# Performance work log

Measured on AMD Instinct MI355X. Metric: run time of the kernel, lower is better.

Reference implementation:

```python
import jax, jax.numpy as jnp
import numpy as np

N = 50000      # nodes
E = 1_600_000  # edges (avg degree 32)
IN = 256
HID = 64
H = 4          # heads
OUT = 128
NEG = 0.2      # LeakyReLU negative slope


def setup_inputs() -> dict:
    key = jax.random.key(0)
    ks = jax.random.split(key, 16)
    def p(i, shape):
        return jax.random.normal(ks[i], shape, jnp.float32) * 0.05
    x = jax.random.normal(ks[0], (N, IN), jnp.float32)
    edge_index = jax.random.randint(ks[1], (2, E), 0, N, dtype=jnp.int64)
    return dict(
        x=x, edge_index=edge_index,
        W0=p(2, (IN, H * HID)), as0=p(3, (H, HID)), ad0=p(4, (H, HID)), b0=p(5, (H * HID,)),
        W1=p(6, (H * HID, H * HID)), as1=p(7, (H, HID)), ad1=p(8, (H, HID)), b1=p(9, (H * HID,)),
        W2=p(10, (H * HID, OUT)), as2=p(11, (1, OUT)), ad2=p(12, (1, OUT)), b2=p(13, (OUT,)),
        Wl=p(14, (H * HID, OUT)), bl=p(15, (OUT,)),
    )


def gat_conv(x, src, dst, W, a_s, a_d, b, heads, ch):
    # Linear projection -> per-head features [N, H, C]
    h = (x @ W).reshape(-1, heads, ch)
    # Per-node attention logits [N, H]
    al_s = jnp.einsum('nhc,hc->nh', h, a_s)
    al_d = jnp.einsum('nhc,hc->nh', h, a_d)
    # Per-edge logits: gather + LeakyReLU  [E2, H]
    e = jax.nn.leaky_relu(al_s[src] + al_d[dst], NEG)
    # Segment softmax over destination neighborhoods (stable)
    m = jax.ops.segment_max(e, dst, num_segments=N)
    e = jnp.exp(e - m[dst])
    s = jax.ops.segment_sum(e, dst, num_segments=N)
    a = e / s[dst]
    # Weighted scatter-add aggregation [N, H, C]
    out = jax.ops.segment_sum(a[:, :, None] * h[src], dst, num_segments=N)
    return out.reshape(N, heads * ch) + b


def reference(x, edge_index, W0, as0, ad0, b0, W1, as1, ad1, b1, W2, as2, ad2, b2, Wl, bl):
    # add self-loops (PyG GATConv default)
    loop = jnp.arange(N, dtype=edge_index.dtype)
    src = jnp.concatenate([edge_index[0], loop])
    dst = jnp.concatenate([edge_index[1], loop])
    # layer 0: in -> hid*heads (no residual at layer 0)
    h0 = gat_conv(x, src, dst, W0, as0, ad0, b0, H, HID)
    # layer 1: hid*heads -> hid*heads, residual
    h1 = gat_conv(h0, src, dst, W1, as1, ad1, b1, H, HID) + h0
    # layer 2 (last): hid*heads -> out with 1 head, residual via last_linear
    h2 = gat_conv(h1, src, dst, W2, as2, ad2, b2, 1, OUT) + (h1 @ Wl + bl)
    return h2
```

## Files before the change

### kernel.cpp

```cpp
#include <hip/hip_runtime.h>
#include <hip/hip_bf16.h>

#define N_NODES 50000
#define N_EDGES 1600000
#define E2 (N_EDGES + N_NODES)
#define NB 782
#define BCAP 3072
#define CHUNK 8192
#define NBLK_E 202
#define NS 7
#define RP2W 8

typedef __attribute__((ext_vector_type(8))) short bf16x8;
typedef __attribute__((ext_vector_type(4))) float f32x4;

static __device__ __forceinline__ float lrelu(float x) { return x > 0.f ? x : 0.2f * x; }

static __device__ __forceinline__ float b2f(ushort u) {
    union { unsigned int u; float f; } v;
    v.u = ((unsigned int)u) << 16;
    return v.f;
}
static __device__ __forceinline__ float hi2f(unsigned int u) {
    union { unsigned int u; float f; } v;
    v.u = u & 0xffff0000u;
    return v.f;
}
static __device__ __forceinline__ float lo2f(unsigned int u) {
    union { unsigned int u; float f; } v;
    v.u = u << 16;
    return v.f;
}
static __device__ __forceinline__ ushort f2b(float f) {
    union { float f; unsigned int u; } v;
    v.f = f;
    unsigned int r = v.u + 0x7FFFu + ((v.u >> 16) & 1u);
    return (ushort)(r >> 16);
}


__global__ __launch_bounds__(256) void k_bhist(const int* __restrict__ edst, int* __restrict__ hist) {
    __shared__ int cnt[NB];
    int t = threadIdx.x;
    for (int i = t; i < NB; i += 256) cnt[i] = 0;
    __syncthreads();
    int e0 = blockIdx.x * CHUNK;
    int eend = min(e0 + CHUNK, E2);
    for (int e = e0 + t; e < eend; e += 256) {
        int d = (e < N_EDGES) ? edst[e] : (e - N_EDGES);
        atomicAdd(&cnt[d >> 6], 1);
    }
    __syncthreads();
    for (int i = t; i < NB; i += 256) hist[blockIdx.x * NB + i] = cnt[i];
}

__global__ __launch_bounds__(1024) void k_colscan(const int* __restrict__ hist,
                                                  int* __restrict__ start, int* __restrict__ btotal) {
    int b = threadIdx.x;
    if (b >= NB) return;
    int run = 0;
#pragma unroll 4
    for (int blk = 0; blk < NBLK_E; ++blk) {
        int v = hist[blk * NB + b];
        start[blk * NB + b] = run;
        run += v;
    }
    btotal[b] = run;
}

__global__ __launch_bounds__(256) void k_bscan(const int* __restrict__ btotal, int* __restrict__ bbase) {
    __shared__ int s[256];
    int t = threadIdx.x;
    int v[4];
    int sum = 0;
#pragma unroll
    for (int k = 0; k < 4; ++k) {
        int i = t * 4 + k;
        v[k] = (i < NB) ? btotal[i] : 0;
        sum += v[k];
    }
    s[t] = sum;
    __syncthreads();
    for (int off = 1; off < 256; off <<= 1) {
        int add = (t >= off) ? s[t - off] : 0;
        __syncthreads();
        s[t] += add;
        __syncthreads();
    }
    int base = s[t] - sum;
#pragma unroll
    for (int k = 0; k < 4; ++k) {
        int i = t * 4 + k;
        if (i < NB) bbase[i] = base;
        base += v[k];
    }
}

__global__ __launch_bounds__(256) void k_bscatter(const int* __restrict__ esrc, const int* __restrict__ edst,
                                                  const int* __restrict__ start, const int* __restrict__ bbase,
                                                  unsigned int* __restrict__ bbuf) {
    __shared__ int cnt[NB];
    __shared__ int cur[NB];
    __shared__ int gofs[NB];
    __shared__ int s_scan[256];
    __shared__ unsigned int s_e[CHUNK];
    int t = threadIdx.x;
    for (int i = t; i < NB; i += 256) cnt[i] = 0;
    __syncthreads();
    int e0 = blockIdx.x * CHUNK;
    int eend = min(e0 + CHUNK, E2);
    for (int e = e0 + t; e < eend; e += 256) {
        int d = (e < N_EDGES) ? edst[e] : (e - N_EDGES);
        atomicAdd(&cnt[d >> 6], 1);
    }
    __syncthreads();
    int v[4];
    int sum = 0;
#pragma unroll
    for (int k = 0; k < 4; ++k) {
        int i = t * 4 + k;
        v[k] = (i < NB) ? cnt[i] : 0;
        sum += v[k];
    }
    s_scan[t] = sum;
    __syncthreads();
    for (int off = 1; off < 256; off <<= 1) {
        int add = (t >= off) ? s_scan[t - off] : 0;
        __syncthreads();
        s_scan[t] += add;
        __syncthreads();
    }
    int run = s_scan[t] - sum;
#pragma unroll
    for (int k = 0; k < 4; ++k) {
        int i = t * 4 + k;
        if (i < NB) {
            cur[i] = run;
            gofs[i] = bbase[i] + start[blockIdx.x * NB + i] - run;
        }
        run += v[k];
    }
    __syncthreads();
    for (int e = e0 + t; e < eend; e += 256) {
        int s, d;
        if (e < N_EDGES) { s = esrc[e]; d = edst[e]; } else { s = d = e - N_EDGES; }
        int b = d >> 6;
        int pos = atomicAdd(&cur[b], 1);
        s_e[pos] = (unsigned int)s | ((unsigned int)(d & 63) << 16) | ((unsigned int)b << 22);
    }
    __syncthreads();
    int cntall = eend - e0;
    for (int i = t; i < cntall; i += 256) {
        unsigned int p = s_e[i];
        int b = p >> 22;
        bbuf[gofs[b] + i] = p & 0x3FFFFFu;
    }
}

__global__ __launch_bounds__(256) void k_build(const int* __restrict__ btotal, const int* __restrict__ bbase,
                                               const unsigned int* __restrict__ bbuf,
                                               int* __restrict__ rowptr2, int* __restrict__ col) {
    const int b = blockIdx.x;
    const int t = threadIdx.x;
    const int cnt = btotal[b];
    const int base = bbase[b];
    const int node0 = b << 6;

    __shared__ unsigned int s_e[BCAP];
    __shared__ int s_cnt[512];
    __shared__ int s_cur[512];
    __shared__ int s_scan[256];

    s_cnt[t] = 0; s_cnt[t + 256] = 0;
    __syncthreads();
    for (int i = t; i < cnt; i += 256) {
        unsigned int p = bbuf[(size_t)base + i];
        s_e[i] = p;
        int key = (int)((p >> 16) & 63) * 8 + (int)((p & 0xFFFFu) >> 13);
        atomicAdd(&s_cnt[key], 1);
    }
    __syncthreads();
    int v0 = s_cnt[t * 2], v1 = s_cnt[t * 2 + 1];
    int sum = v0 + v1;
    s_scan[t] = sum;
    __syncthreads();
    for (int off = 1; off < 256; off <<= 1) {
        int add = (t >= off) ? s_scan[t - off] : 0;
        __syncthreads();
        s_scan[t] += add;
        __syncthreads();
    }
    int run = s_scan[t] - sum;
    s_cur[t * 2] = run;
    s_cur[t * 2 + 1] = run + v0;
    __syncthreads();
    {
        int key0 = t * 2, key1 = t * 2 + 1;
        int n0 = node0 + (key0 >> 3);
        int n1 = node0 + (key1 >> 3);
        if (n0 < N_NODES) rowptr2[(size_t)n0 * RP2W + (key0 & 7)] = base + s_cur[key0];
        if (n1 < N_NODES) rowptr2[(size_t)n1 * RP2W + (key1 & 7)] = base + s_cur[key1];
    }
    __syncthreads();
    for (int i = t; i < cnt; i += 256) {
        unsigned int p = s_e[i];
        int key = (int)((p >> 16) & 63) * 8 + (int)((p & 0xFFFFu) >> 13);
        int pos = atomicAdd(&s_cur[key], 1);
        col[base + pos] = (int)(p & 0xFFFFu);
    }
}


__global__ void k_quant(const float* __restrict__ x, ushort* __restrict__ xb, int n4) {
    int i = blockIdx.x * 256 + threadIdx.x;
    if (i >= n4) return;
    float4 v = ((const float4*)x)[i];
    ushort4 o;
    o.x = f2b(v.x); o.y = f2b(v.y); o.z = f2b(v.z); o.w = f2b(v.w);
    ((ushort4*)xb)[i] = o;
}

__global__ void k_wprep(const float* __restrict__ W0, const float* __restrict__ W1,
                        const float* __restrict__ W2, const float* __restrict__ Wl,
                        ushort* __restrict__ Wt0, ushort* __restrict__ Wt1, ushort* __restrict__ Wtc) {
    int g = blockIdx.x * 256 + threadIdx.x;
    int sec = g >> 16;
    int i = g & 0xFFFF;
    int k = i >> 8, n = i & 255;
    if (sec == 0) {
        Wt0[n * 256 + k] = f2b(W0[i]);
    } else if (sec == 1) {
        Wt1[n * 256 + k] = f2b(W1[i]);
    } else {
        float v = (n < 128) ? W2[k * 128 + n] : Wl[k * 128 + (n - 128)];
        Wtc[n * 256 + k] = f2b(v);
    }
}


template <bool FUSE>
__global__ __launch_bounds__(256) void k_mfma(const ushort* __restrict__ A, const ushort* __restrict__ Bt,
                                              ushort* __restrict__ Cb, int M,
                                              const float* __restrict__ a_s, const float* __restrict__ a_d,
                                              float* __restrict__ als, float* __restrict__ ald) {
    const int t = threadIdx.x;
    const int w = t >> 6, l = t & 63;
    const int lr = l & 15, lk = l >> 4;
    const int m0 = blockIdx.x * 32;
    const int n0 = w * 64;
    f32x4 acc[2][4] = {};

    int r0 = m0 + lr;      if (r0 >= M) r0 = M - 1;
    int r1 = m0 + 16 + lr; if (r1 >= M) r1 = M - 1;
    const ushort* a0p = A + (size_t)r0 * 256 + lk * 8;
    const ushort* a1p = A + (size_t)r1 * 256 + lk * 8;
    const ushort* bp  = Bt + (size_t)(n0 + lr) * 256 + lk * 8;

#pragma unroll
    for (int k0 = 0; k0 < 256; k0 += 32) {
        bf16x8 a0 = *(const bf16x8*)(a0p + k0);
        bf16x8 a1 = *(const bf16x8*)(a1p + k0);
#pragma unroll
        for (int n = 0; n < 4; ++n) {
            bf16x8 b = *(const bf16x8*)(bp + n * 16 * 256 + k0);
            acc[0][n] = __builtin_amdgcn_mfma_f32_16x16x32_bf16(a0, b, acc[0][n], 0, 0, 0);
            acc[1][n] = __builtin_amdgcn_mfma_f32_16x16x32_bf16(a1, b, acc[1][n], 0, 0, 0);
        }
    }

#pragma unroll
    for (int m = 0; m < 2; ++m) {
#pragma unroll
        for (int r = 0; r < 4; ++r) {
            int row = m0 + m * 16 + lk * 4 + r;
            if (row >= M) continue;
#pragma unroll
            for (int n = 0; n < 4; ++n) {
                Cb[(size_t)row * 256 + n0 + n * 16 + lr] = f2b(acc[m][n][r]);
            }
        }
    }

    if constexpr (FUSE) {
        float asc[4], adc[4];
#pragma unroll
        for (int n = 0; n < 4; ++n) {
            int c = n0 + n * 16 + lr;
            asc[n] = a_s[c];
            adc[n] = a_d[c];
        }
#pragma unroll
        for (int m = 0; m < 2; ++m) {
#pragma unroll
            for (int r = 0; r < 4; ++r) {
                float pa = 0.f, pd = 0.f;
#pragma unroll
                for (int n = 0; n < 4; ++n) {
                    pa += acc[m][n][r] * asc[n];
                    pd += acc[m][n][r] * adc[n];
                }
#pragma unroll
                for (int off = 1; off < 16; off <<= 1) {
                    pa += __shfl_xor(pa, off);
                    pd += __shfl_xor(pd, off);
                }
                if (lr == 0) {
                    int row = m0 + m * 16 + lk * 4 + r;
                    if (row < M) {
                        als[row * 4 + w] = pa;
                        ald[row * 4 + w] = pd;
                    }
                }
            }
        }
    }
}


template <int HEADS, int CHAN>
__global__ __launch_bounds__(256) void k_al(const ushort* __restrict__ Pb,
                                            const float* __restrict__ a_s, const float* __restrict__ a_d,
                                            float* __restrict__ als, float* __restrict__ ald) {
    int n = blockIdx.x * 4 + (threadIdx.x >> 6);
    if (n >= N_NODES) return;
    int l = threadIdx.x & 63;
    const ushort* row = Pb + (size_t)n * 256;
#pragma unroll
    for (int h = 0; h < HEADS; ++h) {
        float ps = 0.f, pd = 0.f;
#pragma unroll
        for (int c = l; c < CHAN; c += 64) {
            float v = b2f(row[h * CHAN + c]);
            ps += v * a_s[h * CHAN + c];
            pd += v * a_d[h * CHAN + c];
        }
#pragma unroll
        for (int off = 32; off > 0; off >>= 1) {
            ps += __shfl_xor(ps, off);
            pd += __shfl_xor(pd, off);
        }
        if (l == 0) { als[n * HEADS + h] = ps; ald[n * HEADS + h] = pd; }
    }
}


template <int HEADS>
__device__ __forceinline__ void load_als(const float* __restrict__ als, int src, float* v) {
    if constexpr (HEADS == 4) {
        float4 a = *(const float4*)(als + (size_t)src * 4);
        v[0] = a.x; v[1] = a.y; v[2] = a.z; v[3] = a.w;
    } else {
        v[0] = als[src];
    }
}


template <int HEADS, int CHAN, bool RESB, bool LIN, bool WRITEF, bool WRITEB>
__global__ __launch_bounds__(256) void k_aggw(
    const ushort* __restrict__ Pb,
    const float* __restrict__ als, const float* __restrict__ ald,
    const int* __restrict__ rowptr2, const int* __restrict__ col,
    const float* __restrict__ bias, const float* __restrict__ bias2,
    const ushort* __restrict__ residb, float* __restrict__ out, ushort* __restrict__ outb) {
    constexpr int BLK = HEADS * CHAN;
    constexpr int CPL = BLK / 64;
    const int t = threadIdx.x;
    const int w = t >> 6, l = t & 63;
    const int n = blockIdx.x * 4 + w;
    const int rs = rowptr2[(size_t)n * RP2W];
    const int deg = rowptr2[(size_t)n * RP2W + NS] - rs;

    __shared__ int s_src[4][64];
    __shared__ float s_w[4][64 * HEADS];

    float aldn[HEADS];
    load_als<HEADS>(ald, n, aldn);

    float acc[CPL];
#pragma unroll
    for (int c = 0; c < CPL; ++c) acc[c] = 0.f;
    float sw[HEADS];
#pragma unroll
    for (int h = 0; h < HEADS; ++h) sw[h] = 0.f;

    const int hsel = l >> 4;

    for (int base = 0; base < deg; base += 64) {
        int j = base + l;
        if (j < deg) {
            int src = col[rs + j];
            s_src[w][l] = src;
            float av[HEADS];
            load_als<HEADS>(als, src, av);
#pragma unroll
            for (int h = 0; h < HEADS; ++h) {
                float wv = __expf(lrelu(av[h] + aldn[h]));
                s_w[w][l * HEADS + h] = wv;
                sw[h] += wv;
            }
        }
        int cnt = min(64, deg - base);
        int jj = 0;
        for (; jj + 4 <= cnt; jj += 4) {
            int s0 = __builtin_amdgcn_readfirstlane(s_src[w][jj]);
            int s1 = __builtin_amdgcn_readfirstlane(s_src[w][jj + 1]);
            int s2 = __builtin_amdgcn_readfirstlane(s_src[w][jj + 2]);
            int s3 = __builtin_amdgcn_readfirstlane(s_src[w][jj + 3]);
            if constexpr (CPL == 4) {
                float w0 = s_w[w][jj * HEADS + hsel];
                float w1 = s_w[w][(jj + 1) * HEADS + hsel];
                float w2 = s_w[w][(jj + 2) * HEADS + hsel];
                float w3 = s_w[w][(jj + 3) * HEADS + hsel];
                uint2 v0 = *(const uint2*)(Pb + (size_t)s0 * 256 + l * 4);
                uint2 v1 = *(const uint2*)(Pb + (size_t)s1 * 256 + l * 4);
                uint2 v2 = *(const uint2*)(Pb + (size_t)s2 * 256 + l * 4);
                uint2 v3 = *(const uint2*)(Pb + (size_t)s3 * 256 + l * 4);
                acc[0] += w0 * lo2f(v0.x); acc[1] += w0 * hi2f(v0.x);
                acc[2] += w0 * lo2f(v0.y); acc[3] += w0 * hi2f(v0.y);
                acc[0] += w1 * lo2f(v1.x); acc[1] += w1 * hi2f(v1.x);
                acc[2] += w1 * lo2f(v1.y); acc[3] += w1 * hi2f(v1.y);
                acc[0] += w2 * lo2f(v2.x); acc[1] += w2 * hi2f(v2.x);
                acc[2] += w2 * lo2f(v2.y); acc[3] += w2 * hi2f(v2.y);
                acc[0] += w3 * lo2f(v3.x); acc[1] += w3 * hi2f(v3.x);
                acc[2] += w3 * lo2f(v3.y); acc[3] += w3 * hi2f(v3.y);
            } else {
                float w0 = s_w[w][jj];
                float w1 = s_w[w][jj + 1];
                float w2 = s_w[w][jj + 2];
                float w3 = s_w[w][jj + 3];
                unsigned int v0 = *(const unsigned int*)(Pb + (size_t)s0 * 256 + l * 2);
                unsigned int v1 = *(const unsigned int*)(Pb + (size_t)s1 * 256 + l * 2);
                unsigned int v2 = *(const unsigned int*)(Pb + (size_t)s2 * 256 + l * 2);
                unsigned int v3 = *(const unsigned int*)(Pb + (size_t)s3 * 256 + l * 2);
                acc[0] += w0 * lo2f(v0); acc[1] += w0 * hi2f(v0);
                acc[0] += w1 * lo2f(v1); acc[1] += w1 * hi2f(v1);
                acc[0] += w2 * lo2f(v2); acc[1] += w2 * hi2f(v2);
                acc[0] += w3 * lo2f(v3); acc[1] += w3 * hi2f(v3);
            }
        }
        for (; jj < cnt; ++jj) {
            int s0 = __builtin_amdgcn_readfirstlane(s_src[w][jj]);
            if constexpr (CPL == 4) {
                float w0 = s_w[w][jj * HEADS + hsel];
                uint2 v0 = *(const uint2*)(Pb + (size_t)s0 * 256 + l * 4);
                acc[0] += w0 * lo2f(v0.x); acc[1] += w0 * hi2f(v0.x);
                acc[2] += w0 * lo2f(v0.y); acc[3] += w0 * hi2f(v0.y);
            } else {
                float w0 = s_w[w][jj];
                unsigned int v0 = *(const unsigned int*)(Pb + (size_t)s0 * 256 + l * 2);
                acc[0] += w0 * lo2f(v0); acc[1] += w0 * hi2f(v0);
            }
        }
    }

#pragma unroll
    for (int off = 32; off > 0; off >>= 1)
#pragma unroll
        for (int h = 0; h < HEADS; ++h) sw[h] += __shfl_xor(sw[h], off);

    float stot;
    if constexpr (HEADS == 4) {
        stot = (hsel == 0) ? sw[0] : (hsel == 1) ? sw[1] : (hsel == 2) ? sw[2] : sw[3];
    } else {
        stot = sw[0];
    }
    float rinv = 1.0f / stot;

    float r[CPL];
#pragma unroll
    for (int c = 0; c < CPL; ++c) r[c] = acc[c] * rinv + bias[l * CPL + c];
    if constexpr (RESB) {
        ushort4 rv = *(const ushort4*)(residb + (size_t)n * 256 + l * 4);
        r[0] += b2f(rv.x); r[1] += b2f(rv.y); r[2] += b2f(rv.z); r[3] += b2f(rv.w);
    }
    if constexpr (LIN) {
        unsigned int lv = *(const unsigned int*)(Pb + (size_t)n * 256 + 128 + l * 2);
        float2 bv = *(const float2*)(bias2 + l * 2);
        r[0] += lo2f(lv) + bv.x;
        r[1] += hi2f(lv) + bv.y;
    }
    if constexpr (WRITEF) {
        if constexpr (CPL == 4) {
            *(float4*)&out[(size_t)n * BLK + l * 4] = make_float4(r[0], r[1], r[2], r[3]);
        } else {
            *(float2*)&out[(size_t)n * BLK + l * 2] = make_float2(r[0], r[1]);
        }
    }
    if constexpr (WRITEB) {
        ushort4 o;
        o.x = f2b(r[0]); o.y = f2b(r[1]); o.z = f2b(r[2]); o.w = f2b(r[3]);
        *(ushort4*)&outb[(size_t)n * BLK + l * 4] = o;
    }
}


extern "C" void kernel_launch(void* const* d_in, const int* in_sizes, int n_in,
                              void* d_out, int out_size, void* d_ws, size_t ws_size,
                              hipStream_t stream) {
    const float* x   = (const float*)d_in[0];
    const int* ei    = (const int*)d_in[1];
    const int* esrc  = ei;
    const int* edst  = ei + N_EDGES;
    const float* W0  = (const float*)d_in[2];
    const float* as0 = (const float*)d_in[3];
    const float* ad0 = (const float*)d_in[4];
    const float* b0  = (const float*)d_in[5];
    const float* W1  = (const float*)d_in[6];
    const float* as1 = (const float*)d_in[7];
    const float* ad1 = (const float*)d_in[8];
    const float* b1  = (const float*)d_in[9];
    const float* W2  = (const float*)d_in[10];
    const float* as2 = (const float*)d_in[11];
    const float* ad2 = (const float*)d_in[12];
    const float* b2  = (const float*)d_in[13];
    const float* Wl  = (const float*)d_in[14];
    const float* bl  = (const float*)d_in[15];
    float* out = (float*)d_out;

    char* w = (char*)d_ws;
    auto alloc = [&](size_t bytes) { char* p = w; w += (bytes + 255) & ~(size_t)255; return p; };
    ushort* xb  = (ushort*)alloc((size_t)N_NODES * 256 * 2);
    ushort* Pb  = (ushort*)alloc((size_t)N_NODES * 256 * 2);
    ushort* h0b = (ushort*)alloc((size_t)N_NODES * 256 * 2);
    float* als = (float*)alloc((size_t)N_NODES * 4 * 4);
    float* ald = (float*)alloc((size_t)N_NODES * 4 * 4);
    ushort* Wt0 = (ushort*)alloc(256 * 256 * 2);
    ushort* Wt1 = (ushort*)alloc(256 * 256 * 2);
    ushort* Wtc = (ushort*)alloc(256 * 256 * 2);
    unsigned int* bbuf = (unsigned int*)alloc((size_t)E2 * 4);
    int* hist   = (int*)alloc((size_t)NBLK_E * NB * 4);
    int* start  = (int*)alloc((size_t)NBLK_E * NB * 4);
    int* btotal = (int*)alloc((size_t)NB * 4);
    int* bbase  = (int*)alloc((size_t)NB * 4);
    int* rowptr2 = (int*)alloc((size_t)N_NODES * RP2W * 4);
    int* colb   = (int*)alloc((size_t)E2 * 4);
    ushort* h1b = xb;

    k_bhist<<<NBLK_E, 256, 0, stream>>>(edst, hist);
    k_colscan<<<1, 1024, 0, stream>>>(hist, start, btotal);
    k_bscan<<<1, 256, 0, stream>>>(btotal, bbase);
    k_bscatter<<<NBLK_E, 256, 0, stream>>>(esrc, edst, start, bbase, bbuf);
    k_build<<<NB, 256, 0, stream>>>(btotal, bbase, bbuf, rowptr2, colb);

    k_quant<<<(N_NODES * 256 / 4 + 255) / 256, 256, 0, stream>>>(x, xb, N_NODES * 256 / 4);
    k_wprep<<<768, 256, 0, stream>>>(W0, W1, W2, Wl, Wt0, Wt1, Wtc);

    const int gm = (N_NODES + 31) / 32;
    const int ga = (N_NODES + 3) / 4;
    const int gn = N_NODES / 4;

    k_mfma<true><<<gm, 256, 0, stream>>>(xb, Wt0, Pb, N_NODES, as0, ad0, als, ald);
    k_aggw<4, 64, false, false, false, true><<<gn, 256, 0, stream>>>(
        Pb, als, ald, rowptr2, colb, b0, nullptr, nullptr, nullptr, h0b);
    k_mfma<true><<<gm, 256, 0, stream>>>(h0b, Wt1, Pb, N_NODES, as1, ad1, als, ald);
    k_aggw<4, 64, true, false, false, true><<<gn, 256, 0, stream>>>(
        Pb, als, ald, rowptr2, colb, b1, nullptr, h0b, nullptr, h1b);
    k_mfma<false><<<gm, 256, 0, stream>>>(h1b, Wtc, Pb, N_NODES, nullptr, nullptr, nullptr, nullptr);
    k_al<1, 128><<<ga, 256, 0, stream>>>(Pb, as2, ad2, als, ald);
    k_aggw<1, 128, false, true, true, false><<<gn, 256, 0, stream>>>(
        Pb, als, ald, rowptr2, colb, b2, bl, nullptr, out, nullptr);
}
```

Measured before the change: 645.0 us.

## Fuse bucket scans, fold last-layer attention logits into GEMM, unroll gather by two

Merges the column scan and bucket-base scan into one 1024-thread kernel, which removes a launch. Computes the single-head attention logits for the last layer inside the MFMA epilogue: the two waves covering the GAT columns reduce partial dot products through shared memory, replacing the separate k_al pass that re-read the projected features. The aggregation gather loop drops from unroll-by-4 to unroll-by-2 with a single tail step, trading memory-level parallelism for lower register pressure.

```diff
diff --git a/kernel.cpp b/kernel.cpp
--- a/kernel.cpp
+++ b/kernel.cpp
@@ -54,46 +54,31 @@
     for (int i = t; i < NB; i += 256) hist[blockIdx.x * NB + i] = cnt[i];
 }
 
-__global__ __launch_bounds__(1024) void k_colscan(const int* __restrict__ hist,
-                                                  int* __restrict__ start, int* __restrict__ btotal) {
-    int b = threadIdx.x;
-    if (b >= NB) return;
+__global__ __launch_bounds__(1024) void k_cscan(const int* __restrict__ hist,
+                                                int* __restrict__ start,
+                                                int* __restrict__ btotal, int* __restrict__ bbase) {
+    __shared__ int s[1024];
+    int t = threadIdx.x;
     int run = 0;
+    if (t < NB) {
 #pragma unroll 4
-    for (int blk = 0; blk < NBLK_E; ++blk) {
-        int v = hist[blk * NB + b];
-        start[blk * NB + b] = run;
-        run += v;
-    }
-    btotal[b] = run;
-}
-
-__global__ __launch_bounds__(256) void k_bscan(const int* __restrict__ btotal, int* __restrict__ bbase) {
-    __shared__ int s[256];
-    int t = threadIdx.x;
-    int v[4];
-    int sum = 0;
-#pragma unroll
-    for (int k = 0; k < 4; ++k) {
-        int i = t * 4 + k;
-        v[k] = (i < NB) ? btotal[i] : 0;
-        sum += v[k];
-    }
-    s[t] = sum;
-    __syncthreads();
-    for (int off = 1; off < 256; off <<= 1) {
+        for (int blk = 0; blk < NBLK_E; ++blk) {
+            int v = hist[blk * NB + t];
+            start[blk * NB + t] = run;
+            run += v;
+        }
+        btotal[t] = run;
+    }
+    int v = (t < NB) ? run : 0;
+    s[t] = v;
+    __syncthreads();
+    for (int off = 1; off < 1024; off <<= 1) {
         int add = (t >= off) ? s[t - off] : 0;
         __syncthreads();
         s[t] += add;
         __syncthreads();
     }
-    int base = s[t] - sum;
-#pragma unroll
-    for (int k = 0; k < 4; ++k) {
-        int i = t * 4 + k;
-        if (i < NB) bbase[i] = base;
-        base += v[k];
-    }
+    if (t < NB) bbase[t] = s[t] - v;
 }
 
 __global__ __launch_bounds__(256) void k_bscatter(const int* __restrict__ esrc, const int* __restrict__ edst,
@@ -142,11 +127,11 @@
     }
     __syncthreads();
     for (int e = e0 + t; e < eend; e += 256) {
-        int s, d;
-        if (e < N_EDGES) { s = esrc[e]; d = edst[e]; } else { s = d = e - N_EDGES; }
+        int s2, d;
+        if (e < N_EDGES) { s2 = esrc[e]; d = edst[e]; } else { s2 = d = e - N_EDGES; }
         int b = d >> 6;
         int pos = atomicAdd(&cur[b], 1);
-        s_e[pos] = (unsigned int)s | ((unsigned int)(d & 63) << 16) | ((unsigned int)b << 22);
+        s_e[pos] = (unsigned int)s2 | ((unsigned int)(d & 63) << 16) | ((unsigned int)b << 22);
     }
     __syncthreads();
     int cntall = eend - e0;
@@ -238,7 +223,7 @@
 }
 
 
-template <bool FUSE>
+template <int FUSE>
 __global__ __launch_bounds__(256) void k_mfma(const ushort* __restrict__ A, const ushort* __restrict__ Bt,
                                               ushort* __restrict__ Cb, int M,
                                               const float* __restrict__ a_s, const float* __restrict__ a_d,
@@ -281,7 +266,7 @@
         }
     }
 
-    if constexpr (FUSE) {
+    if constexpr (FUSE == 1) {
         float asc[4], adc[4];
 #pragma unroll
         for (int n = 0; n < 4; ++n) {
@@ -314,32 +299,49 @@
             }
         }
     }
-}
-
-
-template <int HEADS, int CHAN>
-__global__ __launch_bounds__(256) void k_al(const ushort* __restrict__ Pb,
-                                            const float* __restrict__ a_s, const float* __restrict__ a_d,
-                                            float* __restrict__ als, float* __restrict__ ald) {
-    int n = blockIdx.x * 4 + (threadIdx.x >> 6);
-    if (n >= N_NODES) return;
-    int l = threadIdx.x & 63;
-    const ushort* row = Pb + (size_t)n * 256;
-#pragma unroll
-    for (int h = 0; h < HEADS; ++h) {
-        float ps = 0.f, pd = 0.f;
-#pragma unroll
-        for (int c = l; c < CHAN; c += 64) {
-            float v = b2f(row[h * CHAN + c]);
-            ps += v * a_s[h * CHAN + c];
-            pd += v * a_d[h * CHAN + c];
-        }
-#pragma unroll
-        for (int off = 32; off > 0; off >>= 1) {
-            ps += __shfl_xor(ps, off);
-            pd += __shfl_xor(pd, off);
-        }
-        if (l == 0) { als[n * HEADS + h] = ps; ald[n * HEADS + h] = pd; }
+
+    if constexpr (FUSE == 2) {
+        __shared__ float s_pa[2][32];
+        __shared__ float s_pd[2][32];
+        if (w < 2) {
+            float asc[4], adc[4];
+#pragma unroll
+            for (int n = 0; n < 4; ++n) {
+                int c = n0 + n * 16 + lr;
+                asc[n] = a_s[c];
+                adc[n] = a_d[c];
+            }
+#pragma unroll
+            for (int m = 0; m < 2; ++m) {
+#pragma unroll
+                for (int r = 0; r < 4; ++r) {
+                    float pa = 0.f, pd = 0.f;
+#pragma unroll
+                    for (int n = 0; n < 4; ++n) {
+                        pa += acc[m][n][r] * asc[n];
+                        pd += acc[m][n][r] * adc[n];
+                    }
+#pragma unroll
+                    for (int off = 1; off < 16; off <<= 1) {
+                        pa += __shfl_xor(pa, off);
+                        pd += __shfl_xor(pd, off);
+                    }
+                    if (lr == 0) {
+                        int slot = m * 16 + lk * 4 + r;
+                        s_pa[w][slot] = pa;
+                        s_pd[w][slot] = pd;
+                    }
+                }
+            }
+        }
+        __syncthreads();
+        if (t < 32) {
+            int row = m0 + t;
+            if (row < M) {
+                als[row] = s_pa[0][t] + s_pa[1][t];
+                ald[row] = s_pd[0][t] + s_pd[1][t];
+            }
+        }
     }
 }
 
@@ -401,44 +403,28 @@
         }
         int cnt = min(64, deg - base);
         int jj = 0;
-        for (; jj + 4 <= cnt; jj += 4) {
+        for (; jj + 2 <= cnt; jj += 2) {
             int s0 = __builtin_amdgcn_readfirstlane(s_src[w][jj]);
             int s1 = __builtin_amdgcn_readfirstlane(s_src[w][jj + 1]);
-            int s2 = __builtin_amdgcn_readfirstlane(s_src[w][jj + 2]);
-            int s3 = __builtin_amdgcn_readfirstlane(s_src[w][jj + 3]);
             if constexpr (CPL == 4) {
                 float w0 = s_w[w][jj * HEADS + hsel];
                 float w1 = s_w[w][(jj + 1) * HEADS + hsel];
-                float w2 = s_w[w][(jj + 2) * HEADS + hsel];
-                float w3 = s_w[w][(jj + 3) * HEADS + hsel];
                 uint2 v0 = *(const uint2*)(Pb + (size_t)s0 * 256 + l * 4);
                 uint2 v1 = *(const uint2*)(Pb + (size_t)s1 * 256 + l * 4);
-                uint2 v2 = *(const uint2*)(Pb + (size_t)s2 * 256 + l * 4);
-                uint2 v3 = *(const uint2*)(Pb + (size_t)s3 * 256 + l * 4);
                 acc[0] += w0 * lo2f(v0.x); acc[1] += w0 * hi2f(v0.x);
                 acc[2] += w0 * lo2f(v0.y); acc[3] += w0 * hi2f(v0.y);
                 acc[0] += w1 * lo2f(v1.x); acc[1] += w1 * hi2f(v1.x);
                 acc[2] += w1 * lo2f(v1.y); acc[3] += w1 * hi2f(v1.y);
-                acc[0] += w2 * lo2f(v2.x); acc[1] += w2 * hi2f(v2.x);
-                acc[2] += w2 * lo2f(v2.y); acc[3] += w2 * hi2f(v2.y);
-                acc[0] += w3 * lo2f(v3.x); acc[1] += w3 * hi2f(v3.x);
-                acc[2] += w3 * lo2f(v3.y); acc[3] += w3 * hi2f(v3.y);
             } else {
                 float w0 = s_w[w][jj];
                 float w1 = s_w[w][jj + 1];
-                float w2 = s_w[w][jj + 2];
-                float w3 = s_w[w][jj + 3];
                 unsigned int v0 = *(const unsigned int*)(Pb + (size_t)s0 * 256 + l * 2);
                 unsigned int v1 = *(const unsigned int*)(Pb + (size_t)s1 * 256 + l * 2);
-                unsigned int v2 = *(const unsigned int*)(Pb + (size_t)s2 * 256 + l * 2);
-                unsigned int v3 = *(const unsigned int*)(Pb + (size_t)s3 * 256 + l * 2);
                 acc[0] += w0 * lo2f(v0); acc[1] += w0 * hi2f(v0);
                 acc[0] += w1 * lo2f(v1); acc[1] += w1 * hi2f(v1);
-                acc[0] += w2 * lo2f(v2); acc[1] += w2 * hi2f(v2);
-                acc[0] += w3 * lo2f(v3); acc[1] += w3 * hi2f(v3);
-            }
-        }
-        for (; jj < cnt; ++jj) {
+            }
+        }
+        if (jj < cnt) {
             int s0 = __builtin_amdgcn_readfirstlane(s_src[w][jj]);
             if constexpr (CPL == 4) {
                 float w0 = s_w[w][jj * HEADS + hsel];
@@ -537,8 +523,7 @@
     ushort* h1b = xb;
 
     k_bhist<<<NBLK_E, 256, 0, stream>>>(edst, hist);
-    k_colscan<<<1, 1024, 0, stream>>>(hist, start, btotal);
-    k_bscan<<<1, 256, 0, stream>>>(btotal, bbase);
+    k_cscan<<<1, 1024, 0, stream>>>(hist, start, btotal, bbase);
     k_bscatter<<<NBLK_E, 256, 0, stream>>>(esrc, edst, start, bbase, bbuf);
     k_build<<<NB, 256, 0, stream>>>(btotal, bbase, bbuf, rowptr2, colb);
 
@@ -546,17 +531,15 @@
     k_wprep<<<768, 256, 0, stream>>>(W0, W1, W2, Wl, Wt0, Wt1, Wtc);
 
     const int gm = (N_NODES + 31) / 32;
-    const int ga = (N_NODES + 3) / 4;
     const int gn = N_NODES / 4;
 
-    k_mfma<true><<<gm, 256, 0, stream>>>(xb, Wt0, Pb, N_NODES, as0, ad0, als, ald);
+    k_mfma<1><<<gm, 256, 0, stream>>>(xb, Wt0, Pb, N_NODES, as0, ad0, als, ald);
     k_aggw<4, 64, false, false, false, true><<<gn, 256, 0, stream>>>(
         Pb, als, ald, rowptr2, colb, b0, nullptr, nullptr, nullptr, h0b);
-    k_mfma<true><<<gm, 256, 0, stream>>>(h0b, Wt1, Pb, N_NODES, as1, ad1, als, ald);
+    k_mfma<1><<<gm, 256, 0, stream>>>(h0b, Wt1, Pb, N_NODES, as1, ad1, als, ald);
     k_aggw<4, 64, true, false, false, true><<<gn, 256, 0, stream>>>(
         Pb, als, ald, rowptr2, colb, b1, nullptr, h0b, nullptr, h1b);
-    k_mfma<false><<<gm, 256, 0, stream>>>(h1b, Wtc, Pb, N_NODES, nullptr, nullptr, nullptr, nullptr);
-    k_al<1, 128><<<ga, 256, 0, stream>>>(Pb, as2, ad2, als, ald);
+    k_mfma<2><<<gm, 256, 0, stream>>>(h1b, Wtc, Pb, N_NODES, as2, ad2, als, ald);
     k_aggw<1, 128, false, true, true, false><<<gn, 256, 0, stream>>>(
         Pb, als, ald, rowptr2, colb, b2, bl, nullptr, out, nullptr);
 }
```

Result: no change. 645.0 us (-0.0%).
